# Kernel tuning notes

Hardware: AMD Instinct MI355X
Metric: run time of the kernel (lower is better)

The kernel has to match this reference:

```python
import jax, jax.numpy as jnp
import numpy as np

HEADS = 4
DIM_HEAD = 128


def setup_inputs() -> dict:
    key = jax.random.key(0)
    k1, k2, k3 = jax.random.split(key, 3)
    dim = 256
    hidden = HEADS * DIM_HEAD  # 512
    x = jax.random.normal(k1, (16, dim, 64, 64), dtype=jnp.float32)
    # 1x1 conv weights stored as [out_ch, in_ch] (kernel dims squeezed)
    w_qkv = jax.random.normal(k2, (hidden * 3, dim), dtype=jnp.float32) * (1.0 / np.sqrt(dim))
    w_out = jax.random.normal(k3, (dim, hidden), dtype=jnp.float32) * (1.0 / np.sqrt(hidden))
    b_out = jnp.zeros((dim,), dtype=jnp.float32)
    return {"x": x, "w_qkv": w_qkv, "w_out": w_out, "b_out": b_out}


def reference(x, w_qkv, w_out, b_out):
    b, c, h, w = x.shape
    n = h * w
    # 1x1 conv == per-pixel linear projection
    qkv = jnp.einsum('bchw,oc->bohw', x, w_qkv)           # [b, 3*heads*dh, h, w]
    qkv = qkv.reshape(b, 3, HEADS, DIM_HEAD, n)           # 'b (qkv heads c) h w -> qkv b heads c (h w)'
    q, k, v = qkv[:, 0], qkv[:, 1], qkv[:, 2]             # [b, heads, dh, n]
    k = jax.nn.softmax(k, axis=-1)                        # softmax over spatial positions
    context = jnp.einsum('bhdn,bhen->bhde', k, v)         # [b, heads, dh, dh]
    out = jnp.einsum('bhde,bhdn->bhen', context, q)       # [b, heads, dh, n]
    out = out.reshape(b, HEADS * DIM_HEAD, h, w)          # 'b heads c (h w) -> b (heads c) h w'
    y = jnp.einsum('bchw,oc->bohw', out, w_out) + b_out[None, :, None, None]
    return y
```

## Files before the change

### kernel.cpp

```cpp
#include <hip/hip_runtime.h>

#define BATCH 16
#define CIN   256
#define NSP   4096
#define HID   512

typedef short v8s __attribute__((ext_vector_type(8)));
typedef float v4f __attribute__((ext_vector_type(4)));

__device__ __forceinline__ unsigned short f2bf(float f) {
    union { float f; unsigned u; } a; a.f = f;
    unsigned r = a.u + 0x7fffu + ((a.u >> 16) & 1u);
    return (unsigned short)(r >> 16);
}

__device__ __forceinline__ void gld_lds16(const unsigned short* g, unsigned short* l) {
    __builtin_amdgcn_global_load_lds(
        (const __attribute__((address_space(1))) unsigned int*)g,
        (__attribute__((address_space(3))) unsigned int*)l,
        16, 0, 0);
}


__global__ __launch_bounds__(256) void k_prep(const float* __restrict__ x,
                                              const float* __restrict__ wq,
                                              unsigned short* __restrict__ xbf,
                                              unsigned short* __restrict__ xT,
                                              unsigned short* __restrict__ wbf,
                                              unsigned short* __restrict__ wqT,
                                              float* __restrict__ zacc) {
    const int bid = blockIdx.x;
    const int t = threadIdx.x;
    if (bid >= 4320) {
        zacc[(bid - 4320) * 256 + t] = 0.f;
        return;
    }
    if (bid >= 4096) {
        const int wid = bid - 4096;
        if (wid < 192) {
            const int g = wid * 256 + t;
            const float4 f0 = *(const float4*)(wq + (size_t)g * 8);
            const float4 f1 = *(const float4*)(wq + (size_t)g * 8 + 4);
            union { unsigned short s[8]; uint4 u; } p;
            p.s[0] = f2bf(f0.x); p.s[1] = f2bf(f0.y); p.s[2] = f2bf(f0.z); p.s[3] = f2bf(f0.w);
            p.s[4] = f2bf(f1.x); p.s[5] = f2bf(f1.y); p.s[6] = f2bf(f1.z); p.s[7] = f2bf(f1.w);
            *(uint4*)(wbf + (size_t)g * 8) = p.u;
            return;
        }
        __shared__ float tile[64 * 65];
        const int bb = wid - 192;
        const int u0 = (bb & 7) * 64, c0 = (bb >> 3) * 64;
        {
            const int cl = (t & 15) * 4, ul = t >> 4;
            #pragma unroll
            for (int i = 0; i < 4; i++) {
                int u = ul + i * 16;
                const float4 f = *(const float4*)(wq + (size_t)(u0 + u) * CIN + c0 + cl);
                *(float4*)(&tile[u * 65 + cl]) = f;
            }
        }
        __syncthreads();
        {
            const int ul4 = (t & 15) * 4, cl = t >> 4;
            #pragma unroll
            for (int i = 0; i < 4; i++) {
                int c = cl + i * 16;
                union { unsigned short s[4]; uint2 u; } p;
                #pragma unroll
                for (int j = 0; j < 4; j++)
                    p.s[j] = f2bf(tile[(ul4 + j) * 65 + c]);
                *(uint2*)(wqT + (size_t)(c0 + c) * HID + u0 + ul4) = p.u;
            }
        }
        return;
    }
    __shared__ float tile[64 * 65];
    const int n0 = (bid & 63) * 64, c0 = ((bid >> 6) & 3) * 64, bz = bid >> 8;
    const float* xb = x + (size_t)bz * CIN * NSP;
    {
        const int nl = (t & 15) * 4, cl = t >> 4;
        #pragma unroll
        for (int i = 0; i < 4; i++) {
            int c = cl + i * 16;
            const float4 f = *(const float4*)(xb + (size_t)(c0 + c) * NSP + n0 + nl);
            *(float4*)(&tile[c * 65 + nl]) = f;
            union { unsigned short s[4]; uint2 u; } p;
            p.s[0] = f2bf(f.x); p.s[1] = f2bf(f.y); p.s[2] = f2bf(f.z); p.s[3] = f2bf(f.w);
            *(uint2*)(xbf + ((size_t)bz * CIN + c0 + c) * NSP + n0 + nl) = p.u;
        }
    }
    __syncthreads();
    {
        const int cl4 = (t & 15) * 4, nl = t >> 4;
        #pragma unroll
        for (int i = 0; i < 4; i++) {
            int n = nl + i * 16;
            union { unsigned short s[4]; uint2 u; } p;
            #pragma unroll
            for (int j = 0; j < 4; j++)
                p.s[j] = f2bf(tile[(cl4 + j) * 65 + n]);
            *(uint2*)(xT + ((size_t)bz * NSP + n0 + n) * CIN + c0 + cl4) = p.u;
        }
    }
}

__global__ __launch_bounds__(256, 2) void k_ks(const unsigned short* __restrict__ wbf,
                                               const unsigned short* __restrict__ xT,
                                               const unsigned short* __restrict__ xbf,
                                               float* __restrict__ Sp,
                                               float* __restrict__ zacc) {
    __shared__ __align__(16) unsigned short A1s[4][64][64];
    __shared__ __align__(16) unsigned short A2s[256][64];
    __shared__ __align__(16) unsigned short Es[64][64];

    const int t = threadIdx.x;
    const int id = blockIdx.x;
    const int bz = id & 15, dblk = (id >> 4) & 7, nc = id >> 7;
    const int d0 = dblk * 64;
    const int nbase = nc * 1024;
    const int lane = t & 63, wv = t >> 6, quad = lane >> 4, l15 = lane & 15;
    const int srow8 = lane >> 3, sslot = lane & 7;
    const int scol = ((sslot - srow8) & 7) * 8;
    const int sw0 = ((quad + l15) & 7) * 8;
    const int wn = wv & 1, wd1 = wv >> 1;
    const int wc = wv;

    auto STAGE_A1 = [&](int n0s) {
        #pragma unroll
        for (int i = 0; i < 8; i++) {
            const int flat = wv * 8 + i;
            const int kl = flat >> 3, rb = flat & 7;
            gld_lds16(xT + ((size_t)bz * NSP + n0s + rb * 8 + srow8) * CIN + kl * 64 + scol,
                      &A1s[kl][rb * 8][0]);
        }
    };
    auto STAGE_A2 = [&](int n0s) {
        #pragma unroll
        for (int i = 0; i < 8; i++) {
            const int rb = wv * 8 + i;
            gld_lds16(xbf + ((size_t)bz * CIN + rb * 8 + srow8) * NSP + n0s + scol,
                      &A2s[rb * 8][0]);
        }
    };

    {
        #pragma unroll
        for (int i = 0; i < 8; i++) {
            const int flat = wv * 8 + i;
            const int kk = flat >> 3, rb = flat & 7;
            gld_lds16(wbf + (size_t)(512 + d0 + rb * 8 + srow8) * CIN + kk * 64 + scol,
                      &A2s[0][0] + (kk * 64 + rb * 8) * 64);
        }
    }
    __syncthreads();
    v8s Wkf[4][2][2];
    #pragma unroll
    for (int kk = 0; kk < 4; kk++)
        #pragma unroll
        for (int ni = 0; ni < 2; ni++)
            #pragma unroll
            for (int h = 0; h < 2; h++) {
                union { v8s v; uint4 u; } rr;
                rr.u = *(const uint4*)(&A2s[0][0] +
                        (size_t)(kk * 64 + wd1 * 32 + ni * 16 + l15) * 64 + (sw0 ^ (h * 32)));
                Wkf[kk][ni][h] = rr.v;
            }
    __syncthreads();

    v4f acc2[4][4];
    #pragma unroll
    for (int i = 0; i < 4; i++)
        #pragma unroll
        for (int j = 0; j < 4; j++) acc2[i][j] = (v4f)0.f;
    float za[2] = {0.f, 0.f};

    STAGE_A1(nbase);

    for (int nt = 0; nt < 16; nt++) {
        const int n0s = nbase + nt * 64;
        __syncthreads();
        STAGE_A2(n0s);

        v4f acc1[2][2];
        #pragma unroll
        for (int i = 0; i < 2; i++)
            #pragma unroll
            for (int j = 0; j < 2; j++) acc1[i][j] = (v4f)0.f;

        __builtin_amdgcn_s_setprio(1);
        #pragma unroll
        for (int kk = 0; kk < 4; kk++) {
            #pragma unroll
            for (int h = 0; h < 2; h++) {
                v8s af[2];
                #pragma unroll
                for (int mi = 0; mi < 2; mi++) {
                    union { v8s v; uint4 u; } rr;
                    rr.u = *(const uint4*)(&A1s[kk][wn * 32 + mi * 16 + l15][0] + (sw0 ^ (h * 32)));
                    af[mi] = rr.v;
                }
                #pragma unroll
                for (int mi = 0; mi < 2; mi++)
                    #pragma unroll
                    for (int ni = 0; ni < 2; ni++)
                        acc1[mi][ni] = __builtin_amdgcn_mfma_f32_16x16x32_bf16(af[mi], Wkf[kk][ni][h], acc1[mi][ni], 0, 0, 0);
            }
        }
        __builtin_amdgcn_s_setprio(0);

        #pragma unroll
        for (int ni = 0; ni < 2; ni++) {
            const int d = wd1 * 32 + ni * 16 + l15;
            #pragma unroll
            for (int mi = 0; mi < 2; mi++) {
                union { unsigned short s[4]; uint2 u; } p;
                #pragma unroll
                for (int rr = 0; rr < 4; rr++) {
                    float e = __expf(acc1[mi][ni][rr]);
                    za[ni] += e;
                    p.s[rr] = f2bf(e);
                }
                const int slot = (wn * 4 + mi * 2 + (quad >> 1) + d) & 7;
                *(uint2*)(&Es[d][slot * 8 + (quad & 1) * 4]) = p.u;
            }
        }
        __syncthreads();
        if (nt < 15) STAGE_A1(n0s + 64);

        __builtin_amdgcn_s_setprio(1);
        #pragma unroll
        for (int kst = 0; kst < 2; kst++) {
            const int esw = sw0 ^ (kst * 32);
            v8s af[4], bfr[4];
            #pragma unroll
            for (int mi = 0; mi < 4; mi++) {
                union { v8s v; uint4 u; } rr;
                rr.u = *(const uint4*)(&A2s[wc * 64 + mi * 16 + l15][0] + esw);
                af[mi] = rr.v;
            }
            #pragma unroll
            for (int ni = 0; ni < 4; ni++) {
                union { v8s v; uint4 u; } rr;
                rr.u = *(const uint4*)(&Es[ni * 16 + l15][0] + esw);
                bfr[ni] = rr.v;
            }
            #pragma unroll
            for (int mi = 0; mi < 4; mi++)
                #pragma unroll
                for (int ni = 0; ni < 4; ni++)
                    acc2[mi][ni] = __builtin_amdgcn_mfma_f32_16x16x32_bf16(af[mi], bfr[ni], acc2[mi][ni], 0, 0, 0);
        }
        __builtin_amdgcn_s_setprio(0);
    }

    #pragma unroll
    for (int ni = 0; ni < 2; ni++) {
        float z = za[ni];
        z += __shfl_xor(z, 16);
        z += __shfl_xor(z, 32);
        if (quad == 0)
            atomicAdd(&zacc[bz * 512 + d0 + wd1 * 32 + ni * 16 + l15], z);
    }

    const int bh = bz * 4 + (dblk >> 1);
    const int ch = wc >> 1;
    float* outp = Sp + ((size_t)(bh * 2 + ch) * 4 + nc) * 16384;
    #pragma unroll
    for (int ni = 0; ni < 4; ni++) {
        const int dl = (dblk & 1) * 64 + ni * 16 + l15;
        #pragma unroll
        for (int mi = 0; mi < 4; mi++) {
            const int cl = (wc & 1) * 64 + mi * 16 + quad * 4;
            *(v4f*)(outp + dl * 128 + cl) = acc2[mi][ni];
        }
    }
}

__global__ __launch_bounds__(256) void k_sred(const float* __restrict__ Sp,
                                              unsigned short* __restrict__ Sred) {
    const int qv = blockIdx.x * 256 + threadIdx.x;
    const int bh = qv >> 13, r = qv & 8191;
    const int dl = r >> 6, cq6 = r & 63;
    const int ch = cq6 >> 5, clq = cq6 & 31;
    const float* p = Sp + ((size_t)(bh * 2 + ch) * 4) * 16384 + dl * 128 + clq * 4;
    float4 s = *(const float4*)p;
    #pragma unroll
    for (int kc = 1; kc < 4; kc++) {
        const float4 f = *(const float4*)(p + (size_t)kc * 16384);
        s.x += f.x; s.y += f.y; s.z += f.z; s.w += f.w;
    }
    union { unsigned short us[4]; uint2 u; } pk;
    pk.us[0] = f2bf(s.x); pk.us[1] = f2bf(s.y); pk.us[2] = f2bf(s.z); pk.us[3] = f2bf(s.w);
    *(uint2*)(Sred + (size_t)bh * 32768 + dl * 256 + cq6 * 4) = pk.u;
}

__global__ __launch_bounds__(256) void k_redwc(const unsigned short* __restrict__ Sred,
                                               const float* __restrict__ zacc,
                                               const unsigned short* __restrict__ wbf,
                                               const float* __restrict__ w_out,
                                               unsigned short* __restrict__ Wc) {
    __shared__ unsigned short Ds[128 * 136];
    __shared__ float zinv[128];
    const int t = threadIdx.x;
    const int bh = blockIdx.x;  const int b = bh >> 2, h = bh & 3;
    const int lane = t & 63, wv = t >> 6, quad = lane >> 4, l15 = lane & 15;

    if (t < 128) zinv[t] = 1.0f / zacc[b * 512 + h * 128 + t];
    __syncthreads();

    {
        const int wm = (wv & 1) * 64, wn = (wv >> 1) * 64;
        const unsigned short* Sb = Sred + (size_t)bh * 32768;
        const unsigned short* Vb = wbf + (size_t)(1024 + h * 128) * CIN;
        v4f acc[4][4];
        #pragma unroll
        for (int i = 0; i < 4; i++)
            #pragma unroll
            for (int j = 0; j < 4; j++) acc[i][j] = (v4f)0.f;
        for (int kk = 0; kk < CIN; kk += 32) {
            v8s af[4], bfr[4];
            #pragma unroll
            for (int mi = 0; mi < 4; mi++) {
                union { v8s v; uint4 u; } rr;
                rr.u = *(const uint4*)(Sb + (size_t)(wm + mi * 16 + l15) * 256 + kk + quad * 8);
                af[mi] = rr.v;
            }
            #pragma unroll
            for (int ni = 0; ni < 4; ni++) {
                union { v8s v; uint4 u; } rr;
                rr.u = *(const uint4*)(Vb + (size_t)(wn + ni * 16 + l15) * 256 + kk + quad * 8);
                bfr[ni] = rr.v;
            }
            #pragma unroll
            for (int mi = 0; mi < 4; mi++)
                #pragma unroll
                for (int ni = 0; ni < 4; ni++)
                    acc[mi][ni] = __builtin_amdgcn_mfma_f32_16x16x32_bf16(af[mi], bfr[ni], acc[mi][ni], 0, 0, 0);
        }
        float zq[4][4];
        #pragma unroll
        for (int mi = 0; mi < 4; mi++)
            #pragma unroll
            for (int rr = 0; rr < 4; rr++)
                zq[mi][rr] = zinv[wm + mi * 16 + quad * 4 + rr];
        #pragma unroll
        for (int mi = 0; mi < 4; mi++)
            #pragma unroll
            for (int ni = 0; ni < 4; ni++)
                #pragma unroll
                for (int rr = 0; rr < 4; rr++)
                    Ds[(wm + mi * 16 + quad * 4 + rr) * 136 + wn + ni * 16 + l15] =
                        f2bf(acc[mi][ni][rr] * zq[mi][rr]);
    }
    __syncthreads();

    {
        const int wm = wv * 64;
        v4f acc[4][8];
        #pragma unroll
        for (int i = 0; i < 4; i++)
            #pragma unroll
            for (int j = 0; j < 8; j++) acc[i][j] = (v4f)0.f;
        for (int kk = 0; kk < 128; kk += 32) {
            v8s af[4], bfr[8];
            #pragma unroll
            for (int mi = 0; mi < 4; mi++) {
                int o = wm + mi * 16 + l15;
                const float* wp = w_out + (size_t)o * HID + h * 128 + kk + quad * 8;
                float4 f0 = *(const float4*)wp;
                float4 f1 = *(const float4*)(wp + 4);
                union { v8s v; unsigned short s[8]; } r;
                r.s[0] = f2bf(f0.x); r.s[1] = f2bf(f0.y); r.s[2] = f2bf(f0.z); r.s[3] = f2bf(f0.w);
                r.s[4] = f2bf(f1.x); r.s[5] = f2bf(f1.y); r.s[6] = f2bf(f1.z); r.s[7] = f2bf(f1.w);
                af[mi] = r.v;
            }
            #pragma unroll
            for (int ni = 0; ni < 8; ni++) {
                union { v8s v; uint4 u; } r;
                r.u = *(const uint4*)(&Ds[(ni * 16 + l15) * 136 + kk + quad * 8]);
                bfr[ni] = r.v;
            }
            #pragma unroll
            for (int mi = 0; mi < 4; mi++)
                #pragma unroll
                for (int ni = 0; ni < 8; ni++)
                    acc[mi][ni] = __builtin_amdgcn_mfma_f32_16x16x32_bf16(af[mi], bfr[ni], acc[mi][ni], 0, 0, 0);
        }
        #pragma unroll
        for (int ni = 0; ni < 8; ni++) {
            int d = ni * 16 + l15;
            #pragma unroll
            for (int mi = 0; mi < 4; mi++)
                #pragma unroll
                for (int rr = 0; rr < 4; rr++) {
                    int o = wm + mi * 16 + quad * 4 + rr;
                    Wc[((size_t)b * 256 + o) * HID + h * 128 + d] = f2bf(acc[mi][ni][rr]);
                }
        }
    }
}

__global__ __launch_bounds__(256) void k_chain(const unsigned short* __restrict__ Wc,
                                               const unsigned short* __restrict__ wqT,
                                               unsigned short* __restrict__ Weff) {
    __shared__ __align__(16) unsigned short As[128 * 64];
    __shared__ __align__(16) unsigned short Bs[128 * 64];
    const int t = threadIdx.x;
    const int c0 = blockIdx.x * 128, o0 = blockIdx.y * 128, bz = blockIdx.z;
    const int lane = t & 63, wv = t >> 6, quad = lane >> 4, l15 = lane & 15;
    const int wmC = (wv & 1) * 64, wnO = (wv >> 1) * 64;

    const int srow8 = lane >> 3, sslot = lane & 7;
    const int scol = ((sslot - srow8) & 7) * 8;
    const int sw0 = ((quad + l15) & 7) * 8;

    const unsigned short* Ag = wqT + (size_t)(c0 + wv * 32 + srow8) * HID + scol;
    const unsigned short* Bg = Wc + ((size_t)bz * 256 + o0 + wv * 32 + srow8) * HID + scol;
    unsigned short* Al = As + wv * 32 * 64;
    unsigned short* Bl = Bs + wv * 32 * 64;

    v4f acc[4][4];
    #pragma unroll
    for (int i = 0; i < 4; i++)
        #pragma unroll
        for (int j = 0; j < 4; j++) acc[i][j] = (v4f)0.f;

    for (int kk = 0; kk < HID; kk += 64) {
        #pragma unroll
        for (int cc = 0; cc < 4; cc++) {
            gld_lds16(Ag + (size_t)(cc * 8) * HID + kk, Al + cc * 8 * 64);
            gld_lds16(Bg + (size_t)(cc * 8) * HID + kk, Bl + cc * 8 * 64);
        }
        __syncthreads();
        #pragma unroll
        for (int h = 0; h < 2; h++) {
            const int sw = sw0 ^ (h * 32);
            v8s af[4], bfr[4];
            #pragma unroll
            for (int mi = 0; mi < 4; mi++) {
                union { v8s v; uint4 u; } rr;
                rr.u = *(const uint4*)(&As[(wmC + mi * 16 + l15) * 64 + sw]);
                af[mi] = rr.v;
            }
            #pragma unroll
            for (int ni = 0; ni < 4; ni++) {
                union { v8s v; uint4 u; } rr;
                rr.u = *(const uint4*)(&Bs[(wnO + ni * 16 + l15) * 64 + sw]);
                bfr[ni] = rr.v;
            }
            #pragma unroll
            for (int mi = 0; mi < 4; mi++)
                #pragma unroll
                for (int ni = 0; ni < 4; ni++)
                    acc[mi][ni] = __builtin_amdgcn_mfma_f32_16x16x32_bf16(af[mi], bfr[ni], acc[mi][ni], 0, 0, 0);
        }
        __syncthreads();
    }
    #pragma unroll
    for (int ni = 0; ni < 4; ni++) {
        const int o = o0 + wnO + ni * 16 + l15;
        #pragma unroll
        for (int mi = 0; mi < 4; mi++) {
            const int c = c0 + wmC + mi * 16 + quad * 4;
            union { unsigned short s[4]; uint2 u; } p;
            #pragma unroll
            for (int rr = 0; rr < 4; rr++) p.s[rr] = f2bf(acc[mi][ni][rr]);
            *(uint2*)(Weff + ((size_t)bz * 256 + o) * 256 + c) = p.u;
        }
    }
}

__global__ __launch_bounds__(256) void k_y(const unsigned short* __restrict__ Weff,
                                           const unsigned short* __restrict__ xT,
                                           const float* __restrict__ b_out,
                                           float* __restrict__ y) {
    __shared__ __align__(16) unsigned short As[128 * 64];
    __shared__ __align__(16) unsigned short Bs[128 * 64];
    const int t = threadIdx.x;
    const int o0 = blockIdx.x * 128;
    const int n0 = blockIdx.y * 128;
    const int bz = blockIdx.z;
    const int lane = t & 63, wv = t >> 6, quad = lane >> 4, l15 = lane & 15;
    const int wmN = (wv & 1) * 64, wnO = (wv >> 1) * 64;

    const int srow8 = lane >> 3, sslot = lane & 7;
    const int scol = ((sslot - srow8) & 7) * 8;
    const int sw0 = ((quad + l15) & 7) * 8;

    const unsigned short* Ag = xT + ((size_t)bz * NSP + n0 + wv * 32 + srow8) * CIN + scol;
    const unsigned short* Bg = Weff + ((size_t)bz * 256 + o0 + wv * 32 + srow8) * CIN + scol;
    unsigned short* Al = As + wv * 32 * 64;
    unsigned short* Bl = Bs + wv * 32 * 64;

    v4f acc[4][4];
    #pragma unroll
    for (int i = 0; i < 4; i++)
        #pragma unroll
        for (int j = 0; j < 4; j++) acc[i][j] = (v4f)0.f;

    for (int kk = 0; kk < CIN; kk += 64) {
        #pragma unroll
        for (int cc = 0; cc < 4; cc++) {
            gld_lds16(Ag + (size_t)(cc * 8) * CIN + kk, Al + cc * 8 * 64);
            gld_lds16(Bg + (size_t)(cc * 8) * CIN + kk, Bl + cc * 8 * 64);
        }
        __syncthreads();
        #pragma unroll
        for (int h = 0; h < 2; h++) {
            const int sw = sw0 ^ (h * 32);
            v8s af[4], bfr[4];
            #pragma unroll
            for (int mi = 0; mi < 4; mi++) {
                union { v8s v; uint4 u; } rr;
                rr.u = *(const uint4*)(&As[(wmN + mi * 16 + l15) * 64 + sw]);
                af[mi] = rr.v;
            }
            #pragma unroll
            for (int ni = 0; ni < 4; ni++) {
                union { v8s v; uint4 u; } rr;
                rr.u = *(const uint4*)(&Bs[(wnO + ni * 16 + l15) * 64 + sw]);
                bfr[ni] = rr.v;
            }
            #pragma unroll
            for (int mi = 0; mi < 4; mi++)
                #pragma unroll
                for (int ni = 0; ni < 4; ni++)
                    acc[mi][ni] = __builtin_amdgcn_mfma_f32_16x16x32_bf16(af[mi], bfr[ni], acc[mi][ni], 0, 0, 0);
        }
        __syncthreads();
    }
    #pragma unroll
    for (int ni = 0; ni < 4; ni++) {
        const int o = o0 + wnO + ni * 16 + l15;
        const float bias = b_out[o];
        #pragma unroll
        for (int mi = 0; mi < 4; mi++) {
            const int n = n0 + wmN + mi * 16 + quad * 4;
            v4f v = acc[mi][ni];
            v[0] += bias; v[1] += bias; v[2] += bias; v[3] += bias;
            *(v4f*)(y + ((size_t)bz * 256 + o) * NSP + n) = v;
        }
    }
}

extern "C" void kernel_launch(void* const* d_in, const int* in_sizes, int n_in,
                              void* d_out, int out_size, void* d_ws, size_t ws_size,
                              hipStream_t stream) {
    (void)in_sizes; (void)n_in; (void)out_size; (void)ws_size;
    const float* x     = (const float*)d_in[0];
    const float* w_qkv = (const float*)d_in[1];
    const float* w_out = (const float*)d_in[2];
    const float* b_out = (const float*)d_in[3];
    float* y = (float*)d_out;
    char* ws = (char*)d_ws;

    unsigned short* xT   = (unsigned short*)(ws);
    unsigned short* xbf  = (unsigned short*)(ws + 33554432);
    float*          Sp   = (float*)(ws + 134217728);
    float*          zacc = (float*)(ws + 167772160);
    unsigned short* Sred = (unsigned short*)(ws + 167804928);
    unsigned short* Wc   = (unsigned short*)(ws + 171999232);
    unsigned short* Weff = (unsigned short*)(ws + 176193536);
    unsigned short* wbf  = (unsigned short*)(ws + 178290688);
    unsigned short* wqT  = (unsigned short*)(ws + 179077120);

    k_prep <<<dim3(4352),       256, 0, stream>>>(x, w_qkv, xbf, xT, wbf, wqT, zacc);
    k_ks   <<<dim3(512),        256, 0, stream>>>(wbf, xT, xbf, Sp, zacc);
    k_sred <<<dim3(2048),       256, 0, stream>>>(Sp, Sred);
    k_redwc<<<dim3(64),         256, 0, stream>>>(Sred, zacc, wbf, w_out, Wc);
    k_chain<<<dim3(2, 2, 16),   256, 0, stream>>>(Wc, wqT, Weff);
    k_y    <<<dim3(2, 32, 16),  256, 0, stream>>>(Weff, xT, b_out, y);
}
```

Baseline: 226.4 us.

## Replace split-K partial buffer and reduce kernel with atomic accumulation into S

The k_ks kernel now accumulates its context partials straight into a zero-initialised fp32 S buffer with atomicAdd, so the separate k_sred reduction kernel and its partial-buffer round trip are gone. k_redwc converts the fp32 S to bf16 on load. The first GEMM's wave split is also changed so each wave covers 16 rows across all 64 d columns, reusing one A fragment for four MFMAs. In exchange this adds many scalar float atomics, zeroing blocks in k_prep, and non-deterministic summation order.

```diff
diff --git a/kernel.cpp b/kernel.cpp
--- a/kernel.cpp
+++ b/kernel.cpp
@@ -28,9 +28,15 @@
                                               unsigned short* __restrict__ xT,
                                               unsigned short* __restrict__ wbf,
                                               unsigned short* __restrict__ wqT,
-                                              float* __restrict__ zacc) {
+                                              float* __restrict__ zacc,
+                                              float* __restrict__ S) {
     const int bid = blockIdx.x;
     const int t = threadIdx.x;
+    if (bid >= 4352) {
+        float4 z; z.x = 0.f; z.y = 0.f; z.z = 0.f; z.w = 0.f;
+        ((float4*)S)[(size_t)(bid - 4352) * 256 + t] = z;
+        return;
+    }
     if (bid >= 4320) {
         zacc[(bid - 4320) * 256 + t] = 0.f;
         return;
@@ -107,7 +113,7 @@
 __global__ __launch_bounds__(256, 2) void k_ks(const unsigned short* __restrict__ wbf,
                                                const unsigned short* __restrict__ xT,
                                                const unsigned short* __restrict__ xbf,
-                                               float* __restrict__ Sp,
+                                               float* __restrict__ S,
                                                float* __restrict__ zacc) {
     __shared__ __align__(16) unsigned short A1s[4][64][64];
     __shared__ __align__(16) unsigned short A2s[256][64];
@@ -122,7 +128,6 @@
     const int srow8 = lane >> 3, sslot = lane & 7;
     const int scol = ((sslot - srow8) & 7) * 8;
     const int sw0 = ((quad + l15) & 7) * 8;
-    const int wn = wv & 1, wd1 = wv >> 1;
     const int wc = wv;
 
     auto STAGE_A1 = [&](int n0s) {
@@ -153,16 +158,16 @@
         }
     }
     __syncthreads();
-    v8s Wkf[4][2][2];
+    v8s Wkf[4][4][2];
     #pragma unroll
     for (int kk = 0; kk < 4; kk++)
         #pragma unroll
-        for (int ni = 0; ni < 2; ni++)
+        for (int ni = 0; ni < 4; ni++)
             #pragma unroll
             for (int h = 0; h < 2; h++) {
                 union { v8s v; uint4 u; } rr;
                 rr.u = *(const uint4*)(&A2s[0][0] +
-                        (size_t)(kk * 64 + wd1 * 32 + ni * 16 + l15) * 64 + (sw0 ^ (h * 32)));
+                        (size_t)(kk * 64 + ni * 16 + l15) * 64 + (sw0 ^ (h * 32)));
                 Wkf[kk][ni][h] = rr.v;
             }
     __syncthreads();
@@ -172,7 +177,7 @@
     for (int i = 0; i < 4; i++)
         #pragma unroll
         for (int j = 0; j < 4; j++) acc2[i][j] = (v4f)0.f;
-    float za[2] = {0.f, 0.f};
+    float za[4] = {0.f, 0.f, 0.f, 0.f};
 
     STAGE_A1(nbase);
 
@@ -181,48 +186,37 @@
         __syncthreads();
         STAGE_A2(n0s);
 
-        v4f acc1[2][2];
-        #pragma unroll
-        for (int i = 0; i < 2; i++)
-            #pragma unroll
-            for (int j = 0; j < 2; j++) acc1[i][j] = (v4f)0.f;
+        v4f acc1[4];
+        #pragma unroll
+        for (int i = 0; i < 4; i++) acc1[i] = (v4f)0.f;
 
         __builtin_amdgcn_s_setprio(1);
         #pragma unroll
         for (int kk = 0; kk < 4; kk++) {
             #pragma unroll
             for (int h = 0; h < 2; h++) {
-                v8s af[2];
-                #pragma unroll
-                for (int mi = 0; mi < 2; mi++) {
-                    union { v8s v; uint4 u; } rr;
-                    rr.u = *(const uint4*)(&A1s[kk][wn * 32 + mi * 16 + l15][0] + (sw0 ^ (h * 32)));
-                    af[mi] = rr.v;
-                }
-                #pragma unroll
-                for (int mi = 0; mi < 2; mi++)
-                    #pragma unroll
-                    for (int ni = 0; ni < 2; ni++)
-                        acc1[mi][ni] = __builtin_amdgcn_mfma_f32_16x16x32_bf16(af[mi], Wkf[kk][ni][h], acc1[mi][ni], 0, 0, 0);
+                union { v8s v; uint4 u; } rr;
+                rr.u = *(const uint4*)(&A1s[kk][wv * 16 + l15][0] + (sw0 ^ (h * 32)));
+                const v8s af = rr.v;
+                #pragma unroll
+                for (int ni = 0; ni < 4; ni++)
+                    acc1[ni] = __builtin_amdgcn_mfma_f32_16x16x32_bf16(af, Wkf[kk][ni][h], acc1[ni], 0, 0, 0);
             }
         }
         __builtin_amdgcn_s_setprio(0);
 
         #pragma unroll
-        for (int ni = 0; ni < 2; ni++) {
-            const int d = wd1 * 32 + ni * 16 + l15;
-            #pragma unroll
-            for (int mi = 0; mi < 2; mi++) {
-                union { unsigned short s[4]; uint2 u; } p;
-                #pragma unroll
-                for (int rr = 0; rr < 4; rr++) {
-                    float e = __expf(acc1[mi][ni][rr]);
-                    za[ni] += e;
-                    p.s[rr] = f2bf(e);
-                }
-                const int slot = (wn * 4 + mi * 2 + (quad >> 1) + d) & 7;
-                *(uint2*)(&Es[d][slot * 8 + (quad & 1) * 4]) = p.u;
-            }
+        for (int ni = 0; ni < 4; ni++) {
+            const int d = ni * 16 + l15;
+            union { unsigned short s[4]; uint2 u; } p;
+            #pragma unroll
+            for (int rr = 0; rr < 4; rr++) {
+                float e = __expf(acc1[ni][rr]);
+                za[ni] += e;
+                p.s[rr] = f2bf(e);
+            }
+            const int slot = (wv * 2 + (quad >> 1) + d) & 7;
+            *(uint2*)(&Es[d][slot * 8 + (quad & 1) * 4]) = p.u;
         }
         __syncthreads();
         if (nt < 15) STAGE_A1(n0s + 64);
@@ -254,47 +248,32 @@
     }
 
     #pragma unroll
-    for (int ni = 0; ni < 2; ni++) {
+    for (int ni = 0; ni < 4; ni++) {
         float z = za[ni];
         z += __shfl_xor(z, 16);
         z += __shfl_xor(z, 32);
         if (quad == 0)
-            atomicAdd(&zacc[bz * 512 + d0 + wd1 * 32 + ni * 16 + l15], z);
+            atomicAdd(&zacc[bz * 512 + d0 + ni * 16 + l15], z);
     }
 
     const int bh = bz * 4 + (dblk >> 1);
-    const int ch = wc >> 1;
-    float* outp = Sp + ((size_t)(bh * 2 + ch) * 4 + nc) * 16384;
+    float* Sb = S + (size_t)bh * 32768;
     #pragma unroll
     for (int ni = 0; ni < 4; ni++) {
         const int dl = (dblk & 1) * 64 + ni * 16 + l15;
         #pragma unroll
         for (int mi = 0; mi < 4; mi++) {
-            const int cl = (wc & 1) * 64 + mi * 16 + quad * 4;
-            *(v4f*)(outp + dl * 128 + cl) = acc2[mi][ni];
-        }
-    }
-}
-
-__global__ __launch_bounds__(256) void k_sred(const float* __restrict__ Sp,
-                                              unsigned short* __restrict__ Sred) {
-    const int qv = blockIdx.x * 256 + threadIdx.x;
-    const int bh = qv >> 13, r = qv & 8191;
-    const int dl = r >> 6, cq6 = r & 63;
-    const int ch = cq6 >> 5, clq = cq6 & 31;
-    const float* p = Sp + ((size_t)(bh * 2 + ch) * 4) * 16384 + dl * 128 + clq * 4;
-    float4 s = *(const float4*)p;
-    #pragma unroll
-    for (int kc = 1; kc < 4; kc++) {
-        const float4 f = *(const float4*)(p + (size_t)kc * 16384);
-        s.x += f.x; s.y += f.y; s.z += f.z; s.w += f.w;
-    }
-    union { unsigned short us[4]; uint2 u; } pk;
-    pk.us[0] = f2bf(s.x); pk.us[1] = f2bf(s.y); pk.us[2] = f2bf(s.z); pk.us[3] = f2bf(s.w);
-    *(uint2*)(Sred + (size_t)bh * 32768 + dl * 256 + cq6 * 4) = pk.u;
-}
-
-__global__ __launch_bounds__(256) void k_redwc(const unsigned short* __restrict__ Sred,
+            const int cl = (wc >> 1) * 128 + (wc & 1) * 64 + mi * 16 + quad * 4;
+            float* rp = Sb + (size_t)dl * 256 + cl;
+            atomicAdd(rp + 0, acc2[mi][ni][0]);
+            atomicAdd(rp + 1, acc2[mi][ni][1]);
+            atomicAdd(rp + 2, acc2[mi][ni][2]);
+            atomicAdd(rp + 3, acc2[mi][ni][3]);
+        }
+    }
+}
+
+__global__ __launch_bounds__(256) void k_redwc(const float* __restrict__ S,
                                                const float* __restrict__ zacc,
                                                const unsigned short* __restrict__ wbf,
                                                const float* __restrict__ w_out,
@@ -310,7 +289,7 @@
 
     {
         const int wm = (wv & 1) * 64, wn = (wv >> 1) * 64;
-        const unsigned short* Sb = Sred + (size_t)bh * 32768;
+        const float* Sb = S + (size_t)bh * 32768;
         const unsigned short* Vb = wbf + (size_t)(1024 + h * 128) * CIN;
         v4f acc[4][4];
         #pragma unroll
@@ -321,9 +300,13 @@
             v8s af[4], bfr[4];
             #pragma unroll
             for (int mi = 0; mi < 4; mi++) {
-                union { v8s v; uint4 u; } rr;
-                rr.u = *(const uint4*)(Sb + (size_t)(wm + mi * 16 + l15) * 256 + kk + quad * 8);
-                af[mi] = rr.v;
+                const float* rp = Sb + (size_t)(wm + mi * 16 + l15) * 256 + kk + quad * 8;
+                const float4 f0 = *(const float4*)rp;
+                const float4 f1 = *(const float4*)(rp + 4);
+                union { v8s v; unsigned short s[8]; } r;
+                r.s[0] = f2bf(f0.x); r.s[1] = f2bf(f0.y); r.s[2] = f2bf(f0.z); r.s[3] = f2bf(f0.w);
+                r.s[4] = f2bf(f1.x); r.s[5] = f2bf(f1.y); r.s[6] = f2bf(f1.z); r.s[7] = f2bf(f1.w);
+                af[mi] = r.v;
             }
             #pragma unroll
             for (int ni = 0; ni < 4; ni++) {
@@ -556,18 +539,16 @@
 
     unsigned short* xT   = (unsigned short*)(ws);
     unsigned short* xbf  = (unsigned short*)(ws + 33554432);
-    float*          Sp   = (float*)(ws + 134217728);
-    float*          zacc = (float*)(ws + 167772160);
-    unsigned short* Sred = (unsigned short*)(ws + 167804928);
-    unsigned short* Wc   = (unsigned short*)(ws + 171999232);
-    unsigned short* Weff = (unsigned short*)(ws + 176193536);
-    unsigned short* wbf  = (unsigned short*)(ws + 178290688);
-    unsigned short* wqT  = (unsigned short*)(ws + 179077120);
-
-    k_prep <<<dim3(4352),       256, 0, stream>>>(x, w_qkv, xbf, xT, wbf, wqT, zacc);
-    k_ks   <<<dim3(512),        256, 0, stream>>>(wbf, xT, xbf, Sp, zacc);
-    k_sred <<<dim3(2048),       256, 0, stream>>>(Sp, Sred);
-    k_redwc<<<dim3(64),         256, 0, stream>>>(Sred, zacc, wbf, w_out, Wc);
+    float*          S    = (float*)(ws + 67108864);
+    float*          zacc = (float*)(ws + 75497472);
+    unsigned short* Wc   = (unsigned short*)(ws + 75530240);
+    unsigned short* Weff = (unsigned short*)(ws + 79724544);
+    unsigned short* wbf  = (unsigned short*)(ws + 81821696);
+    unsigned short* wqT  = (unsigned short*)(ws + 82608128);
+
+    k_prep <<<dim3(6400),       256, 0, stream>>>(x, w_qkv, xbf, xT, wbf, wqT, zacc, S);
+    k_ks   <<<dim3(512),        256, 0, stream>>>(wbf, xT, xbf, S, zacc);
+    k_redwc<<<dim3(64),         256, 0, stream>>>(S, zacc, wbf, w_out, Wc);
     k_chain<<<dim3(2, 2, 16),   256, 0, stream>>>(Wc, wqT, Weff);
     k_y    <<<dim3(2, 32, 16),  256, 0, stream>>>(Weff, xT, b_out, y);
 }
```

Result: slower. 326.2 us (+44.1%).
